# Performance work log

Hardware: AMD Instinct MI355X
Metric: run time of the kernel (lower is better)

Reference implementation:

```python
import jax, jax.numpy as jnp
import numpy as np

NUM_RBF = 16
TOP_K = 30
MAX_REL = 32  # max_relative_feature
EPS_D = 1e-6
LN_EPS = 1e-5


def _rbf(D):
    # D: [..., ] -> [..., NUM_RBF]
    mu = jnp.linspace(2.0, 22.0, NUM_RBF)
    sigma = (22.0 - 2.0) / NUM_RBF
    return jnp.exp(-(((D[..., None] - mu) / sigma) ** 2))


def _gather_nb(coords, E_idx):
    # coords: [B,L,3], E_idx: [B,L,K] -> [B,L,K,3]
    return jax.vmap(lambda c, i: c[i])(coords, E_idx)


def reference(X, mask, residue_idx, chain_labels, pe_w, pe_b, edge_w, ln_g, ln_b):
    B, L = X.shape[0], X.shape[1]
    N = X[:, :, 0, :]
    C = X[:, :, 1, :]
    Ca = X[:, :, 2, :]
    O = X[:, :, 3, :]
    # virtual C-beta
    b = Ca - N
    c = C - Ca
    a = jnp.cross(b, c)
    Cb = -0.58273431 * a + 0.56802827 * b - 0.54067466 * c + Ca

    # kNN over masked pairwise C-C distances
    mask2 = mask[:, None, :] * mask[:, :, None]  # [B,L,L]
    dX = C[:, None, :, :] - C[:, :, None, :]
    D = mask2 * jnp.sqrt(jnp.sum(dX ** 2, -1) + EPS_D)
    D_max = jnp.max(D, -1, keepdims=True)
    D_adjust = D + (1.0 - mask2) * D_max
    k = min(TOP_K, L)
    neg_vals, E_idx = jax.lax.top_k(-D_adjust, k)  # smallest distances
    D_neighbors = -neg_vals  # [B,L,K]

    # 25 RBF feature sets: first is the masked topk distance, then 24 atom pairs
    atoms = {'N': N, 'C': C, 'Ca': Ca, 'Cb': Cb, 'O': O}
    pairs = [('N','N'),('Ca','Ca'),('Cb','Cb'),('C','N'),('C','Ca'),('C','Cb'),
             ('N','Ca'),('N','Cb'),('Cb','Ca'),('N','C'),('Ca','C'),('Cb','C'),
             ('Ca','N'),('Cb','N'),('Ca','Cb'),('O','O'),('C','O'),('O','C'),
             ('N','O'),('O','N'),('Cb','O'),('O','Ca'),('O','Cb'),('Ca','O')]
    A_stack = jnp.stack([atoms[p[0]] for p in pairs], 0)  # [P,B,L,3]
    B_stack = jnp.stack([atoms[p[1]] for p in pairs], 0)  # [P,B,L,3]
    Bn = jax.vmap(lambda cb: _gather_nb(cb, E_idx))(B_stack)  # [P,B,L,K,3]
    D_pairs = jnp.sqrt(jnp.sum((A_stack[:, :, :, None, :] - Bn) ** 2, -1) + EPS_D)  # [P,B,L,K]
    RBF_pairs = _rbf(D_pairs)  # [P,B,L,K,R]
    P = len(pairs)
    RBF_pairs = jnp.moveaxis(RBF_pairs, 0, 3).reshape(B, L, k, P * NUM_RBF)
    RBF_all = jnp.concatenate([_rbf(D_neighbors), RBF_pairs], -1)  # [B,L,K,400]

    # positional encodings (relative residue offset gathered at neighbors)
    offset = residue_idx[:, :, None] - residue_idx[:, None, :]  # [B,L,L]
    offset = jnp.take_along_axis(offset, E_idx, axis=2)  # [B,L,K]
    d_chains = (chain_labels[:, :, None] - chain_labels[:, None, :] == 0).astype(jnp.int32)
    E_chains = jnp.take_along_axis(d_chains, E_idx, axis=2)  # [B,L,K]
    d = jnp.clip(offset + MAX_REL, 0, 2 * MAX_REL) * E_chains + (1 - E_chains) * (2 * MAX_REL + 1)
    E_positional = pe_w[d] + pe_b  # one-hot @ W == row gather; [B,L,K,16]

    E = jnp.concatenate([E_positional, RBF_all], -1)  # [B,L,K,416]
    E = E @ edge_w  # [B,L,K,128]
    mu = jnp.mean(E, -1, keepdims=True)
    var = jnp.mean((E - mu) ** 2, -1, keepdims=True)
    E = (E - mu) / jnp.sqrt(var + LN_EPS) * ln_g + ln_b
    return E, E_idx


def setup_inputs() -> dict:
    key = jax.random.key(0)
    ks = jax.random.split(key, 6)
    B, L = 4, 2048
    X = jax.random.normal(ks[0], (B, L, 4, 3), dtype=jnp.float32)
    mask = jnp.ones((B, L), dtype=jnp.float32)
    residue_idx = jnp.arange(B * L, dtype=jnp.int32).reshape(B, L)
    chain_labels = jnp.zeros((B, L), dtype=jnp.int32)
    pe_w = jax.random.normal(ks[1], (66, 16), dtype=jnp.float32) * 0.1
    pe_b = jax.random.normal(ks[2], (16,), dtype=jnp.float32) * 0.1
    edge_w = jax.random.normal(ks[3], (416, 128), dtype=jnp.float32) * 0.05
    ln_g = jnp.ones((128,), dtype=jnp.float32)
    ln_b = jnp.zeros((128,), dtype=jnp.float32)
    return {"X": X, "mask": mask, "residue_idx": residue_idx, "chain_labels": chain_labels,
            "pe_w": pe_w, "pe_b": pe_b, "edge_w": edge_w, "ln_g": ln_g, "ln_b": ln_b}
```

## Files before the change

### kernel.cpp

```cpp
#include <hip/hip_runtime.h>
#include <hip/hip_bf16.h>
#include <cstdint>
#include <cstddef>

#define Bc 4
#define Lc 2048
#define Kc 30
#define Fc 416
#define Nc 128

typedef __bf16 bf16x8 __attribute__((ext_vector_type(8)));
typedef float  f32x4  __attribute__((ext_vector_type(4)));
typedef unsigned short ushortx8 __attribute__((ext_vector_type(8)));

__constant__ int c_pa[24] = {0,2,3,1,1,1,0,0,3,0,2,3,2,3,2,4,1,4,0,4,3,4,4,2};
__constant__ int c_pb[24] = {0,2,3,0,2,3,2,3,2,1,1,1,0,0,3,4,4,1,4,0,4,2,3,2};

__device__ __forceinline__ unsigned long long u64min(unsigned long long a, unsigned long long b) {
    return a < b ? a : b;
}
__device__ __forceinline__ unsigned long long u64max(unsigned long long a, unsigned long long b) {
    return a > b ? a : b;
}

__device__ __forceinline__ unsigned short f2bf(float f) {
    __hip_bfloat16 h = __float2bfloat16(f);
    return *(unsigned short*)&h;
}

__device__ __forceinline__ void rbf8(float d, float mu0, float* v) {
    const float u0 = (d - mu0) * 0.8f;
    v[0] = __expf(-u0 * u0);
    float rr = __expf(fmaf(2.1333333f, u0, -1.1377778f));
    #pragma unroll
    for (int m = 1; m < 8; ++m) {
        v[m] = v[m - 1] * rr;
        rr *= 0.10274083f;
    }
}

__global__ __launch_bounds__(256) void prep_all(const float* __restrict__ Wg,
                                                const float* __restrict__ X,
                                                const float* __restrict__ mask,
                                                unsigned short* __restrict__ Wt,
                                                float4* __restrict__ Cpk) {
    const int blk = blockIdx.x;
    if (blk < 208) {
        const int id = blk * 256 + threadIdx.x;
        const int n = id / Fc, k = id - n * Fc;
        Wt[id] = f2bf(Wg[k * Nc + n]);
    } else {
        const int id = (blk - 208) * 256 + threadIdx.x;
        float4 o;
        o.x = X[(size_t)id * 12 + 3];
        o.y = X[(size_t)id * 12 + 4];
        o.z = X[(size_t)id * 12 + 5];
        o.w = mask[id];
        Cpk[id] = o;
    }
}

__global__ __launch_bounds__(256) void topk3(
    const float4* __restrict__ Cpk,
    int* __restrict__ eidx, float* __restrict__ dnb, float* __restrict__ outEidx)
{
#pragma clang fp contract(off)
    __shared__ unsigned long long pairs[4][256];
    __shared__ int scnt[4];
    const int t = threadIdx.x;
    const int lane = t & 63, wv = t >> 6;
    const int row = blockIdx.x * 4 + wv;

    if (lane == 0) scnt[wv] = 0;

    const float4 ci = Cpk[row];
    const float cix = ci.x, ciy = ci.y, ciz = ci.z, mi = ci.w;
    const float4* base = Cpk + (row & ~(Lc - 1));

    float D[32], am[32];
    float dmax = -1e30f;
    #pragma unroll 8
    for (int s = 0; s < 32; ++s) {
        const float4 f4 = base[s * 64 + lane];
        const float dx = f4.x - cix;
        const float dy = f4.y - ciy;
        const float dz = f4.z - ciz;
        const float ss = dx * dx + dy * dy + dz * dz;
        const float dist = sqrtf(ss + 1e-6f);
        const float m2 = mi * f4.w;
        D[s] = m2 * dist;
        am[s] = 1.0f - m2;
        dmax = fmaxf(dmax, D[s]);
    }
    #pragma unroll
    for (int off = 32; off; off >>= 1) dmax = fmaxf(dmax, __shfl_xor(dmax, off, 64));

    unsigned uv[32];
    unsigned long long lmin = ~0ULL;
    #pragma unroll 8
    for (int s = 0; s < 32; ++s) {
        const float Dadj = D[s] + am[s] * dmax;
        uv[s] = __float_as_uint(Dadj);
        const unsigned long long k =
            ((unsigned long long)uv[s] << 32) | (unsigned)(s * 64 + lane);
        lmin = u64min(lmin, k);
    }

    unsigned long long sv = lmin;
    #pragma unroll
    for (int k = 2; k <= 64; k <<= 1) {
        #pragma unroll
        for (int j = k >> 1; j > 0; j >>= 1) {
            const unsigned long long o =
                (unsigned long long)__shfl_xor((long long)sv, j, 64);
            const bool takeMin = (((lane & k) == 0) == ((lane & j) == 0));
            sv = takeMin ? u64min(sv, o) : u64max(sv, o);
        }
    }
    const unsigned long long Tkey =
        (unsigned long long)__shfl((long long)sv, 29, 64);

    #pragma unroll 8
    for (int s = 0; s < 32; ++s) {
        const unsigned long long key =
            ((unsigned long long)uv[s] << 32) | (unsigned)(s * 64 + lane);
        if (key <= Tkey) {
            const int pos = atomicAdd(&scnt[wv], 1);
            if (pos < 256) pairs[wv][pos] = key;
        }
    }
    const int S = min(scnt[wv], 256);

    for (int p = lane; p < S; p += 64) {
        const unsigned long long kp = pairs[wv][p];
        int r = 0;
        for (int q = 0; q < S; ++q)
            r += (pairs[wv][q] < kp) ? 1 : 0;
        if (r < Kc) {
            const int j = (int)(kp & 0xffffffffULL);
            eidx[row * Kc + r] = j;
            dnb[row * Kc + r] = __uint_as_float((unsigned)(kp >> 32));
            outEidx[(size_t)row * Kc + r] = (float)j;
        }
    }
}

__global__ __launch_bounds__(256) void edge_mfma3(
    const float* __restrict__ X, const int* __restrict__ ridx, const int* __restrict__ clab,
    const float* __restrict__ pe_w, const float* __restrict__ pe_b,
    const unsigned short* __restrict__ Wt,
    const float* __restrict__ ln_g, const float* __restrict__ ln_b,
    const int* __restrict__ eidx, const float* __restrict__ dnb,
    float* __restrict__ outE)
{
    __shared__ unsigned short Bs[2][8][512];
    __shared__ float atomsA[4][17];
    __shared__ float atomsB[120][17];
    __shared__ float dnb_s[120];
    __shared__ int   pid_s[120];

    const int blk = blockIdx.x;
    const int t   = threadIdx.x;
    const int lane = t & 63, w = t >> 6;
    const int b   = blk >> 9;
    const int cl  = lane & 15, q = lane >> 4;

    if (t < 124) {
        int j, rowi = 0;
        float* dst;
        if (t < 120) {
            const int r = t / 30;
            rowi = blk * 4 + r;
            j = eidx[rowi * Kc + (t - r * 30)];
            dst = &atomsB[t][0];
            dnb_s[t] = dnb[rowi * Kc + (t - r * 30)];
            const int off = ridx[rowi] - ridx[b * Lc + j];
            const int ec  = (clab[rowi] == clab[b * Lc + j]) ? 1 : 0;
            pid_s[t] = ec ? min(max(off + 32, 0), 64) : 65;
        } else {
            j = (blk * 4 + (t - 120)) & (Lc - 1);
            dst = &atomsA[t - 120][0];
        }
        const float* p = X + (size_t)(b * Lc + j) * 12;
        const float Nx = p[0],  Ny = p[1],  Nz = p[2];
        const float Cx = p[3],  Cy = p[4],  Cz = p[5];
        const float Cax = p[6], Cay = p[7], Caz = p[8];
        const float Ox = p[9],  Oy = p[10], Oz = p[11];
        const float bx = Cax - Nx, by = Cay - Ny, bz = Caz - Nz;
        const float cx = Cx - Cax, cy = Cy - Cay, cz = Cz - Caz;
        const float ax = by * cz - bz * cy;
        const float ay = bz * cx - bx * cz;
        const float az = bx * cy - by * cx;
        dst[0] = Nx;  dst[1] = Ny;  dst[2] = Nz;
        dst[3] = Cx;  dst[4] = Cy;  dst[5] = Cz;
        dst[6] = Cax; dst[7] = Cay; dst[8] = Caz;
        dst[9]  = -0.58273431f * ax + 0.56802827f * bx - 0.54067466f * cx + Cax;
        dst[10] = -0.58273431f * ay + 0.56802827f * by - 0.54067466f * cy + Cay;
        dst[11] = -0.58273431f * az + 0.56802827f * bz - 0.54067466f * cz + Caz;
        dst[12] = Ox; dst[13] = Oy; dst[14] = Oz;
    }

    const int wrow0 = w * 16 + cl;
    const int wrow1 = (w + 4) * 16 + cl;
    const int wcol  = q * 8;
    const unsigned short* gW0 = Wt + wrow0 * Fc + wcol;
    const unsigned short* gW1 = Wt + wrow1 * Fc + wcol;

    {
        ushortx8 p0 = *(const ushortx8*)gW0;
        ushortx8 p1 = *(const ushortx8*)gW1;
        *(ushortx8*)&Bs[0][w][lane * 8]     = p0;
        *(ushortx8*)&Bs[0][w + 4][lane * 8] = p1;
    }
    __syncthreads();

    f32x4 acc[2][8];
    #pragma unroll
    for (int m = 0; m < 2; ++m)
        #pragma unroll
        for (int n = 0; n < 8; ++n) acc[m][n] = (f32x4){0.f, 0.f, 0.f, 0.f};

    const int row0 = w * 32 + cl;
    const int row1 = row0 + 16;
    const int e0 = min(row0, 119), e1 = min(row1, 119);
    const int r0 = e0 / 30,        r1 = e1 / 30;

    auto afrag = [&](int kc, int e, int r) -> bf16x8 {
        float v[8];
        if (kc == 0) {
            if (q < 2) {
                const int base = pid_s[e] * 16 + q * 8;
                const float4 p0 = *(const float4*)&pe_w[base];
                const float4 p1 = *(const float4*)&pe_w[base + 4];
                const float4 b0 = *(const float4*)&pe_b[q * 8];
                const float4 b1 = *(const float4*)&pe_b[q * 8 + 4];
                v[0] = p0.x + b0.x; v[1] = p0.y + b0.y;
                v[2] = p0.z + b0.z; v[3] = p0.w + b0.w;
                v[4] = p1.x + b1.x; v[5] = p1.y + b1.y;
                v[6] = p1.z + b1.z; v[7] = p1.w + b1.w;
            } else {
                rbf8(dnb_s[e], (q == 2) ? 2.0f : 12.6666667f, v);
            }
        } else {
            const int p  = 2 * kc - 2 + (q >> 1);
            const int a_ = c_pa[p], b_ = c_pb[p];
            const float dx = atomsA[r][a_ * 3 + 0] - atomsB[e][b_ * 3 + 0];
            const float dy = atomsA[r][a_ * 3 + 1] - atomsB[e][b_ * 3 + 1];
            const float dz = atomsA[r][a_ * 3 + 2] - atomsB[e][b_ * 3 + 2];
            const float d = sqrtf(dx * dx + dy * dy + dz * dz + 1e-6f);
            rbf8(d, (q & 1) ? 12.6666667f : 2.0f, v);
        }
        ushortx8 o;
        #pragma unroll
        for (int m = 0; m < 8; ++m) o[m] = f2bf(v[m]);
        return __builtin_bit_cast(bf16x8, o);
    };

    bf16x8 a0c = afrag(0, e0, r0);
    bf16x8 a1c = afrag(0, e1, r1);

    for (int kc = 0; kc < 13; ++kc) {
        const int cur = kc & 1;
        ushortx8 st0, st1;
        bf16x8 a0n, a1n;
        if (kc < 12) {
            st0 = *(const ushortx8*)(gW0 + (kc + 1) * 32);
            st1 = *(const ushortx8*)(gW1 + (kc + 1) * 32);
            a0n = afrag(kc + 1, e0, r0);
            a1n = afrag(kc + 1, e1, r1);
        }
        #pragma unroll
        for (int n = 0; n < 8; ++n) {
            bf16x8 bf = __builtin_bit_cast(bf16x8,
                *(const ushortx8*)&Bs[cur][n][lane * 8]);
            acc[0][n] = __builtin_amdgcn_mfma_f32_16x16x32_bf16(a0c, bf, acc[0][n], 0, 0, 0);
            acc[1][n] = __builtin_amdgcn_mfma_f32_16x16x32_bf16(a1c, bf, acc[1][n], 0, 0, 0);
        }
        if (kc < 12) {
            *(ushortx8*)&Bs[cur ^ 1][w][lane * 8]     = st0;
            *(ushortx8*)&Bs[cur ^ 1][w + 4][lane * 8] = st1;
        }
        __syncthreads();
        a0c = a0n; a1c = a1n;
    }

    float gcol[8], bcol[8];
    #pragma unroll
    for (int n = 0; n < 8; ++n) {
        gcol[n] = ln_g[n * 16 + cl];
        bcol[n] = ln_b[n * 16 + cl];
    }
    #pragma unroll
    for (int m = 0; m < 2; ++m) {
        #pragma unroll
        for (int reg = 0; reg < 4; ++reg) {
            const int rl = w * 32 + m * 16 + q * 4 + reg;
            float s1 = 0.f, s2 = 0.f;
            #pragma unroll
            for (int n = 0; n < 8; ++n) {
                const float v = acc[m][n][reg];
                s1 += v; s2 += v * v;
            }
            #pragma unroll
            for (int off = 1; off < 16; off <<= 1) {
                s1 += __shfl_xor(s1, off, 64);
                s2 += __shfl_xor(s2, off, 64);
            }
            if (rl < 120) {
                const float mu = s1 * (1.0f / 128.0f);
                const float var = s2 * (1.0f / 128.0f) - mu * mu;
                const float rstd = rsqrtf(var + 1e-5f);
                const size_t base = ((size_t)(blk * 120 + rl)) * 128 + cl;
                #pragma unroll
                for (int n = 0; n < 8; ++n) {
                    outE[base + n * 16] =
                        (acc[m][n][reg] - mu) * rstd * gcol[n] + bcol[n];
                }
            }
        }
    }
}

extern "C" void kernel_launch(void* const* d_in, const int* in_sizes, int n_in,
                              void* d_out, int out_size, void* d_ws, size_t ws_size,
                              hipStream_t stream) {
    const float* X     = (const float*)d_in[0];
    const float* mask  = (const float*)d_in[1];
    const int*   ridx  = (const int*)d_in[2];
    const int*   clab  = (const int*)d_in[3];
    const float* pe_w  = (const float*)d_in[4];
    const float* pe_b  = (const float*)d_in[5];
    const float* edge_w = (const float*)d_in[6];
    const float* ln_g  = (const float*)d_in[7];
    const float* ln_b  = (const float*)d_in[8];

    float* outE   = (float*)d_out;
    float* outIdx = outE + (size_t)Bc * Lc * Kc * Nc;

    char* ws = (char*)d_ws;
    int*   eidx = (int*)ws;
    float* dnbw = (float*)(ws + 983040);
    unsigned short* Wt = (unsigned short*)(ws + 1966080);
    float4* Cpk = (float4*)(ws + 2072576);

    prep_all<<<240, 256, 0, stream>>>(edge_w, X, mask, Wt, Cpk);
    topk3<<<Bc * Lc / 4, 256, 0, stream>>>(Cpk, eidx, dnbw, outIdx);
    edge_mfma3<<<Bc * Lc / 4, 256, 0, stream>>>(X, ridx, clab, pe_w, pe_b, Wt,
                                                ln_g, ln_b, eidx, dnbw, outE);
}
```

Measured before the change: 109.6 us.

## Fuse top-k neighbor selection into edge MFMA kernel and use DPP row reductions

Merges the top-k kernel into the edge-feature kernel, since both use the same 4-rows-per-block mapping. Neighbor indices and distances now pass through shared memory instead of a global workspace round trip, and one launch is removed. The top-k part recomputes distances instead of holding 32-entry register arrays, and sorts 32-bit keys instead of 64-bit ones (ties resolved at collection). The LayerNorm 16-lane sums switch from shuffles to DPP row operations; the larger shared footprint and register pressure may reduce occupancy.

```diff
diff --git a/kernel.cpp b/kernel.cpp
--- a/kernel.cpp
+++ b/kernel.cpp
@@ -15,13 +15,6 @@
 
 __constant__ int c_pa[24] = {0,2,3,1,1,1,0,0,3,0,2,3,2,3,2,4,1,4,0,4,3,4,4,2};
 __constant__ int c_pb[24] = {0,2,3,0,2,3,2,3,2,1,1,1,0,0,3,4,4,1,4,0,4,2,3,2};
-
-__device__ __forceinline__ unsigned long long u64min(unsigned long long a, unsigned long long b) {
-    return a < b ? a : b;
-}
-__device__ __forceinline__ unsigned long long u64max(unsigned long long a, unsigned long long b) {
-    return a > b ? a : b;
-}
 
 __device__ __forceinline__ unsigned short f2bf(float f) {
     __hip_bfloat16 h = __float2bfloat16(f);
@@ -37,6 +30,19 @@
         v[m] = v[m - 1] * rr;
         rr *= 0.10274083f;
     }
+}
+
+template<int CTRL>
+__device__ __forceinline__ float dpp_radd(float x) {
+    const int r = __builtin_amdgcn_update_dpp(0, __float_as_int(x), CTRL, 0xf, 0xf, true);
+    return x + __int_as_float(r);
+}
+__device__ __forceinline__ float row16_sum(float x) {
+    x = dpp_radd<0x121>(x);
+    x = dpp_radd<0x122>(x);
+    x = dpp_radd<0x124>(x);
+    x = dpp_radd<0x128>(x);
+    return x;
 }
 
 __global__ __launch_bounds__(256) void prep_all(const float* __restrict__ Wg,
@@ -60,103 +66,21 @@
     }
 }
 
-__global__ __launch_bounds__(256) void topk3(
+__global__ __launch_bounds__(256) void fused_kernel(
     const float4* __restrict__ Cpk,
-    int* __restrict__ eidx, float* __restrict__ dnb, float* __restrict__ outEidx)
-{
-#pragma clang fp contract(off)
-    __shared__ unsigned long long pairs[4][256];
-    __shared__ int scnt[4];
-    const int t = threadIdx.x;
-    const int lane = t & 63, wv = t >> 6;
-    const int row = blockIdx.x * 4 + wv;
-
-    if (lane == 0) scnt[wv] = 0;
-
-    const float4 ci = Cpk[row];
-    const float cix = ci.x, ciy = ci.y, ciz = ci.z, mi = ci.w;
-    const float4* base = Cpk + (row & ~(Lc - 1));
-
-    float D[32], am[32];
-    float dmax = -1e30f;
-    #pragma unroll 8
-    for (int s = 0; s < 32; ++s) {
-        const float4 f4 = base[s * 64 + lane];
-        const float dx = f4.x - cix;
-        const float dy = f4.y - ciy;
-        const float dz = f4.z - ciz;
-        const float ss = dx * dx + dy * dy + dz * dz;
-        const float dist = sqrtf(ss + 1e-6f);
-        const float m2 = mi * f4.w;
-        D[s] = m2 * dist;
-        am[s] = 1.0f - m2;
-        dmax = fmaxf(dmax, D[s]);
-    }
-    #pragma unroll
-    for (int off = 32; off; off >>= 1) dmax = fmaxf(dmax, __shfl_xor(dmax, off, 64));
-
-    unsigned uv[32];
-    unsigned long long lmin = ~0ULL;
-    #pragma unroll 8
-    for (int s = 0; s < 32; ++s) {
-        const float Dadj = D[s] + am[s] * dmax;
-        uv[s] = __float_as_uint(Dadj);
-        const unsigned long long k =
-            ((unsigned long long)uv[s] << 32) | (unsigned)(s * 64 + lane);
-        lmin = u64min(lmin, k);
-    }
-
-    unsigned long long sv = lmin;
-    #pragma unroll
-    for (int k = 2; k <= 64; k <<= 1) {
-        #pragma unroll
-        for (int j = k >> 1; j > 0; j >>= 1) {
-            const unsigned long long o =
-                (unsigned long long)__shfl_xor((long long)sv, j, 64);
-            const bool takeMin = (((lane & k) == 0) == ((lane & j) == 0));
-            sv = takeMin ? u64min(sv, o) : u64max(sv, o);
-        }
-    }
-    const unsigned long long Tkey =
-        (unsigned long long)__shfl((long long)sv, 29, 64);
-
-    #pragma unroll 8
-    for (int s = 0; s < 32; ++s) {
-        const unsigned long long key =
-            ((unsigned long long)uv[s] << 32) | (unsigned)(s * 64 + lane);
-        if (key <= Tkey) {
-            const int pos = atomicAdd(&scnt[wv], 1);
-            if (pos < 256) pairs[wv][pos] = key;
-        }
-    }
-    const int S = min(scnt[wv], 256);
-
-    for (int p = lane; p < S; p += 64) {
-        const unsigned long long kp = pairs[wv][p];
-        int r = 0;
-        for (int q = 0; q < S; ++q)
-            r += (pairs[wv][q] < kp) ? 1 : 0;
-        if (r < Kc) {
-            const int j = (int)(kp & 0xffffffffULL);
-            eidx[row * Kc + r] = j;
-            dnb[row * Kc + r] = __uint_as_float((unsigned)(kp >> 32));
-            outEidx[(size_t)row * Kc + r] = (float)j;
-        }
-    }
-}
-
-__global__ __launch_bounds__(256) void edge_mfma3(
     const float* __restrict__ X, const int* __restrict__ ridx, const int* __restrict__ clab,
     const float* __restrict__ pe_w, const float* __restrict__ pe_b,
     const unsigned short* __restrict__ Wt,
     const float* __restrict__ ln_g, const float* __restrict__ ln_b,
-    const int* __restrict__ eidx, const float* __restrict__ dnb,
-    float* __restrict__ outE)
+    float* __restrict__ outE, float* __restrict__ outEidx)
 {
+    __shared__ unsigned long long pairs[4][256];
+    __shared__ int scnt[4];
     __shared__ unsigned short Bs[2][8][512];
     __shared__ float atomsA[4][17];
     __shared__ float atomsB[120][17];
     __shared__ float dnb_s[120];
+    __shared__ int   jn_s[120];
     __shared__ int   pid_s[120];
 
     const int blk = blockIdx.x;
@@ -164,18 +88,99 @@
     const int lane = t & 63, w = t >> 6;
     const int b   = blk >> 9;
     const int cl  = lane & 15, q = lane >> 4;
+    const int row = blk * 4 + w;
+
+    const unsigned short* gW0 = Wt + (w * 16 + cl) * Fc + q * 8;
+    const unsigned short* gW1 = Wt + ((w + 4) * 16 + cl) * Fc + q * 8;
+    {
+        ushortx8 p0 = *(const ushortx8*)gW0;
+        ushortx8 p1 = *(const ushortx8*)gW1;
+        *(ushortx8*)&Bs[0][w][lane * 8]     = p0;
+        *(ushortx8*)&Bs[0][w + 4][lane * 8] = p1;
+    }
+
+    {
+#pragma clang fp contract(off)
+        if (lane == 0) scnt[w] = 0;
+        const float4 ci = Cpk[row];
+        const float cix = ci.x, ciy = ci.y, ciz = ci.z, mi = ci.w;
+        const float4* basep = Cpk + (row & ~(Lc - 1));
+
+        float dmax = -1e30f;
+        #pragma unroll 8
+        for (int s = 0; s < 32; ++s) {
+            const float4 f4 = basep[s * 64 + lane];
+            const float dx = f4.x - cix, dy = f4.y - ciy, dz = f4.z - ciz;
+            const float dist = sqrtf(dx * dx + dy * dy + dz * dz + 1e-6f);
+            const float D = (mi * f4.w) * dist;
+            dmax = fmaxf(dmax, D);
+        }
+        #pragma unroll
+        for (int off = 32; off; off >>= 1) dmax = fmaxf(dmax, __shfl_xor(dmax, off, 64));
+
+        auto dadjbits = [&](int s) -> unsigned {
+            const float4 f4 = basep[s * 64 + lane];
+            const float dx = f4.x - cix, dy = f4.y - ciy, dz = f4.z - ciz;
+            const float dist = sqrtf(dx * dx + dy * dy + dz * dz + 1e-6f);
+            const float m2 = mi * f4.w;
+            const float D = m2 * dist;
+            const float Dadj = D + (1.0f - m2) * dmax;
+            return __float_as_uint(Dadj);
+        };
+
+        unsigned lmin = 0xffffffffu;
+        #pragma unroll 8
+        for (int s = 0; s < 32; ++s) lmin = min(lmin, dadjbits(s));
+
+        unsigned sv = lmin;
+        #pragma unroll
+        for (int k = 2; k <= 64; k <<= 1) {
+            #pragma unroll
+            for (int j = k >> 1; j > 0; j >>= 1) {
+                const unsigned o = (unsigned)__shfl_xor((int)sv, j, 64);
+                const bool takeMin = (((lane & k) == 0) == ((lane & j) == 0));
+                sv = takeMin ? min(sv, o) : max(sv, o);
+            }
+        }
+        const unsigned Tval = (unsigned)__shfl((int)sv, 29, 64);
+
+        #pragma unroll 8
+        for (int s = 0; s < 32; ++s) {
+            const unsigned u = dadjbits(s);
+            if (u <= Tval) {
+                const int pos = atomicAdd(&scnt[w], 1);
+                if (pos < 256)
+                    pairs[w][pos] =
+                        ((unsigned long long)u << 32) | (unsigned)(s * 64 + lane);
+            }
+        }
+        const int S = min(scnt[w], 256);
+
+        for (int p = lane; p < S; p += 64) {
+            const unsigned long long kp = pairs[w][p];
+            int r = 0;
+            for (int qq = 0; qq < S; ++qq)
+                r += (pairs[w][qq] < kp) ? 1 : 0;
+            if (r < Kc) {
+                const int j = (int)(kp & 0xffffffffULL);
+                jn_s[w * Kc + r]  = j;
+                dnb_s[w * Kc + r] = __uint_as_float((unsigned)(kp >> 32));
+                outEidx[(size_t)row * Kc + r] = (float)j;
+            }
+        }
+    }
+    __syncthreads();
 
     if (t < 124) {
-        int j, rowi = 0;
+        int j;
         float* dst;
         if (t < 120) {
-            const int r = t / 30;
-            rowi = blk * 4 + r;
-            j = eidx[rowi * Kc + (t - r * 30)];
+            j = jn_s[t];
             dst = &atomsB[t][0];
-            dnb_s[t] = dnb[rowi * Kc + (t - r * 30)];
-            const int off = ridx[rowi] - ridx[b * Lc + j];
-            const int ec  = (clab[rowi] == clab[b * Lc + j]) ? 1 : 0;
+            const int rowi = blk * 4 + t / 30;
+            const int jg = b * Lc + j;
+            const int off = ridx[rowi] - ridx[jg];
+            const int ec  = (clab[rowi] == clab[jg]) ? 1 : 0;
             pid_s[t] = ec ? min(max(off + 32, 0), 64) : 65;
         } else {
             j = (blk * 4 + (t - 120)) & (Lc - 1);
@@ -199,19 +204,6 @@
         dst[11] = -0.58273431f * az + 0.56802827f * bz - 0.54067466f * cz + Caz;
         dst[12] = Ox; dst[13] = Oy; dst[14] = Oz;
     }
-
-    const int wrow0 = w * 16 + cl;
-    const int wrow1 = (w + 4) * 16 + cl;
-    const int wcol  = q * 8;
-    const unsigned short* gW0 = Wt + wrow0 * Fc + wcol;
-    const unsigned short* gW1 = Wt + wrow1 * Fc + wcol;
-
-    {
-        ushortx8 p0 = *(const ushortx8*)gW0;
-        ushortx8 p1 = *(const ushortx8*)gW1;
-        *(ushortx8*)&Bs[0][w][lane * 8]     = p0;
-        *(ushortx8*)&Bs[0][w + 4][lane * 8] = p1;
-    }
     __syncthreads();
 
     f32x4 acc[2][8];
@@ -301,11 +293,8 @@
                 const float v = acc[m][n][reg];
                 s1 += v; s2 += v * v;
             }
-            #pragma unroll
-            for (int off = 1; off < 16; off <<= 1) {
-                s1 += __shfl_xor(s1, off, 64);
-                s2 += __shfl_xor(s2, off, 64);
-            }
+            s1 = row16_sum(s1);
+            s2 = row16_sum(s2);
             if (rl < 120) {
                 const float mu = s1 * (1.0f / 128.0f);
                 const float var = s2 * (1.0f / 128.0f) - mu * mu;
@@ -338,13 +327,10 @@
     float* outIdx = outE + (size_t)Bc * Lc * Kc * Nc;
 
     char* ws = (char*)d_ws;
-    int*   eidx = (int*)ws;
-    float* dnbw = (float*)(ws + 983040);
-    unsigned short* Wt = (unsigned short*)(ws + 1966080);
-    float4* Cpk = (float4*)(ws + 2072576);
+    unsigned short* Wt = (unsigned short*)ws;
+    float4* Cpk = (float4*)(ws + 106496);
 
     prep_all<<<240, 256, 0, stream>>>(edge_w, X, mask, Wt, Cpk);
-    topk3<<<Bc * Lc / 4, 256, 0, stream>>>(Cpk, eidx, dnbw, outIdx);
-    edge_mfma3<<<Bc * Lc / 4, 256, 0, stream>>>(X, ridx, clab, pe_w, pe_b, Wt,
-                                                ln_g, ln_b, eidx, dnbw, outE);
-}
+    fused_kernel<<<Bc * Lc / 4, 256, 0, stream>>>(Cpk, X, ridx, clab, pe_w, pe_b,
+                                                  Wt, ln_g, ln_b, outE, outIdx);
+}
```

New measurement: 125.1 us. +14.1%, slower.

## Load weight fragments directly from global memory, drop LDS staging and barriers

Applied to the files above, without the earlier changes.

The edge GEMM kernel no longer stages weight tiles through double-buffered shared memory with a block barrier each K step. Each wave now loads its 8 B fragments straight from global memory (expected to be served from cache) every iteration. The LayerNorm row reductions switch from shfl_xor to DPP row-rotate adds, and launch bounds now request 4 blocks per CU for occupancy. This removes barriers and LDS traffic but multiplies global/L2 weight reads per block by the number of waves and adds register pressure from the 8 in-flight fragments.

```diff
diff --git a/kernel.cpp b/kernel.cpp
--- a/kernel.cpp
+++ b/kernel.cpp
@@ -37,6 +37,19 @@
         v[m] = v[m - 1] * rr;
         rr *= 0.10274083f;
     }
+}
+
+template<int CTRL>
+__device__ __forceinline__ float dpp_radd(float x) {
+    const int r = __builtin_amdgcn_update_dpp(0, __float_as_int(x), CTRL, 0xf, 0xf, true);
+    return x + __int_as_float(r);
+}
+__device__ __forceinline__ float row16_sum(float x) {
+    x = dpp_radd<0x121>(x);
+    x = dpp_radd<0x122>(x);
+    x = dpp_radd<0x124>(x);
+    x = dpp_radd<0x128>(x);
+    return x;
 }
 
 __global__ __launch_bounds__(256) void prep_all(const float* __restrict__ Wg,
@@ -145,7 +158,7 @@
     }
 }
 
-__global__ __launch_bounds__(256) void edge_mfma3(
+__global__ __launch_bounds__(256, 4) void edge_mfma4(
     const float* __restrict__ X, const int* __restrict__ ridx, const int* __restrict__ clab,
     const float* __restrict__ pe_w, const float* __restrict__ pe_b,
     const unsigned short* __restrict__ Wt,
@@ -153,7 +166,6 @@
     const int* __restrict__ eidx, const float* __restrict__ dnb,
     float* __restrict__ outE)
 {
-    __shared__ unsigned short Bs[2][8][512];
     __shared__ float atomsA[4][17];
     __shared__ float atomsB[120][17];
     __shared__ float dnb_s[120];
@@ -166,16 +178,16 @@
     const int cl  = lane & 15, q = lane >> 4;
 
     if (t < 124) {
-        int j, rowi = 0;
+        int j;
         float* dst;
         if (t < 120) {
-            const int r = t / 30;
-            rowi = blk * 4 + r;
-            j = eidx[rowi * Kc + (t - r * 30)];
+            j = eidx[(blk * 4 + t / 30) * Kc + (t % 30)];
             dst = &atomsB[t][0];
-            dnb_s[t] = dnb[rowi * Kc + (t - r * 30)];
-            const int off = ridx[rowi] - ridx[b * Lc + j];
-            const int ec  = (clab[rowi] == clab[b * Lc + j]) ? 1 : 0;
+            dnb_s[t] = dnb[(blk * 4 + t / 30) * Kc + (t % 30)];
+            const int rowi = blk * 4 + t / 30;
+            const int jg = b * Lc + j;
+            const int off = ridx[rowi] - ridx[jg];
+            const int ec  = (clab[rowi] == clab[jg]) ? 1 : 0;
             pid_s[t] = ec ? min(max(off + 32, 0), 64) : 65;
         } else {
             j = (blk * 4 + (t - 120)) & (Lc - 1);
@@ -199,20 +211,12 @@
         dst[11] = -0.58273431f * az + 0.56802827f * bz - 0.54067466f * cz + Caz;
         dst[12] = Ox; dst[13] = Oy; dst[14] = Oz;
     }
-
-    const int wrow0 = w * 16 + cl;
-    const int wrow1 = (w + 4) * 16 + cl;
-    const int wcol  = q * 8;
-    const unsigned short* gW0 = Wt + wrow0 * Fc + wcol;
-    const unsigned short* gW1 = Wt + wrow1 * Fc + wcol;
-
-    {
-        ushortx8 p0 = *(const ushortx8*)gW0;
-        ushortx8 p1 = *(const ushortx8*)gW1;
-        *(ushortx8*)&Bs[0][w][lane * 8]     = p0;
-        *(ushortx8*)&Bs[0][w + 4][lane * 8] = p1;
-    }
     __syncthreads();
+
+    const unsigned short* gBn[8];
+    #pragma unroll
+    for (int n = 0; n < 8; ++n)
+        gBn[n] = Wt + (n * 16 + cl) * Fc + q * 8;
 
     f32x4 acc[2][8];
     #pragma unroll
@@ -260,27 +264,21 @@
     bf16x8 a1c = afrag(0, e1, r1);
 
     for (int kc = 0; kc < 13; ++kc) {
-        const int cur = kc & 1;
-        ushortx8 st0, st1;
+        ushortx8 bf[8];
+        #pragma unroll
+        for (int n = 0; n < 8; ++n)
+            bf[n] = *(const ushortx8*)(gBn[n] + kc * 32);
         bf16x8 a0n, a1n;
         if (kc < 12) {
-            st0 = *(const ushortx8*)(gW0 + (kc + 1) * 32);
-            st1 = *(const ushortx8*)(gW1 + (kc + 1) * 32);
             a0n = afrag(kc + 1, e0, r0);
             a1n = afrag(kc + 1, e1, r1);
         }
         #pragma unroll
         for (int n = 0; n < 8; ++n) {
-            bf16x8 bf = __builtin_bit_cast(bf16x8,
-                *(const ushortx8*)&Bs[cur][n][lane * 8]);
-            acc[0][n] = __builtin_amdgcn_mfma_f32_16x16x32_bf16(a0c, bf, acc[0][n], 0, 0, 0);
-            acc[1][n] = __builtin_amdgcn_mfma_f32_16x16x32_bf16(a1c, bf, acc[1][n], 0, 0, 0);
-        }
-        if (kc < 12) {
-            *(ushortx8*)&Bs[cur ^ 1][w][lane * 8]     = st0;
-            *(ushortx8*)&Bs[cur ^ 1][w + 4][lane * 8] = st1;
-        }
-        __syncthreads();
+            const bf16x8 bb = __builtin_bit_cast(bf16x8, bf[n]);
+            acc[0][n] = __builtin_amdgcn_mfma_f32_16x16x32_bf16(a0c, bb, acc[0][n], 0, 0, 0);
+            acc[1][n] = __builtin_amdgcn_mfma_f32_16x16x32_bf16(a1c, bb, acc[1][n], 0, 0, 0);
+        }
         a0c = a0n; a1c = a1n;
     }
 
@@ -301,11 +299,8 @@
                 const float v = acc[m][n][reg];
                 s1 += v; s2 += v * v;
             }
-            #pragma unroll
-            for (int off = 1; off < 16; off <<= 1) {
-                s1 += __shfl_xor(s1, off, 64);
-                s2 += __shfl_xor(s2, off, 64);
-            }
+            s1 = row16_sum(s1);
+            s2 = row16_sum(s2);
             if (rl < 120) {
                 const float mu = s1 * (1.0f / 128.0f);
                 const float var = s2 * (1.0f / 128.0f) - mu * mu;
@@ -345,6 +340,6 @@
 
     prep_all<<<240, 256, 0, stream>>>(edge_w, X, mask, Wt, Cpk);
     topk3<<<Bc * Lc / 4, 256, 0, stream>>>(Cpk, eidx, dnbw, outIdx);
-    edge_mfma3<<<Bc * Lc / 4, 256, 0, stream>>>(X, ridx, clab, pe_w, pe_b, Wt,
+    edge_mfma4<<<Bc * Lc / 4, 256, 0, stream>>>(X, ridx, clab, pe_w, pe_b, Wt,
                                                 ln_g, ln_b, eidx, dnbw, outE);
 }
```

Measured after the change: 121.1 us. 1.1x slower.
